# Performance work log

Hardware: AMD Instinct MI355X
Metric: run time of the kernel (lower is better)

The kernel has to match this reference:

```python
import jax, jax.numpy as jnp
import numpy as np

SMOOTH_COEF = 0.025
FLOOR = 1e-06
B, T, C = 64, 4096, 128


def setup_inputs() -> dict:
    key = jax.random.key(0)
    k1, = jax.random.split(key, 1)
    inputs = jax.random.uniform(k1, (B, T, C), dtype=jnp.float32)  # nonneg spectrogram-like
    alpha = jnp.full((C,), 0.98, dtype=jnp.float32)
    delta = jnp.full((C,), 2.0, dtype=jnp.float32)
    root = jnp.full((C,), 2.0, dtype=jnp.float32)
    return {"inputs": inputs, "alpha": alpha, "delta": delta, "root": root}


def _ema(x, s):
    # m_t = s*x_t + (1-s)*m_{t-1}, with h_{-1} = x_0 => m_0 = x_0.
    # Linear recurrence via associative scan: pairs (a_t, b_t), m_t = a_t*m_{t-1} + b_t.
    Bn, Tn, Cn = x.shape
    a = jnp.full((Tn,), 1.0 - s, dtype=x.dtype).at[0].set(0.0)
    a = jnp.broadcast_to(a[None, :, None], x.shape)
    b = (s * x).at[:, 0, :].set(x[:, 0, :])

    def comb(c1, c2):
        a1, b1 = c1
        a2, b2 = c2
        return (a1 * a2, a2 * b1 + b2)

    _, m = jax.lax.associative_scan(comb, (a, b), axis=1)
    return m


def reference(inputs, alpha, delta, root):
    alpha_c = jnp.minimum(alpha, 1.0)          # [C]
    root_c = jnp.maximum(root, 1.0)            # [C]
    m = _ema(inputs, SMOOTH_COEF)              # [B,T,C] EMA smoother
    one_over_root = 1.0 / root_c
    term1 = jnp.power(FLOOR + m, alpha_c)
    term2 = jnp.power(inputs / term1 + delta, one_over_root)
    term3 = jnp.power(delta, one_over_root)
    return term2 - term3
```

## Files before the change

kernel.cpp:

```cpp
#include <hip/hip_runtime.h>


constexpr int Bn = 64, Tn = 4096, Cn = 128;
constexpr int L = 256;
constexpr int H = 256;
constexpr int NC = Tn / L;
constexpr int RS = Cn / 2;
constexpr float SC  = 0.025f;
constexpr float OMS = 1.0f - SC;
constexpr float FLOORV = 1e-6f;

__device__ __forceinline__ float pcen1(float x, float m, float al, float dl,
                                       float oor, float t3) {
    float inv1 = exp2f(-al * log2f(FLOORV + m));
    float base = fmaf(x, inv1, dl);
    return exp2f(oor * log2f(base)) - t3;
}

__global__ __launch_bounds__(256) void k_pcen(const float* __restrict__ x,
                                              const float* __restrict__ alpha,
                                              const float* __restrict__ delta,
                                              const float* __restrict__ root,
                                              float* __restrict__ out) {
    int gid   = blockIdx.x * 256 + threadIdx.x;
    int cg    = gid & 63;
    int chunk = (gid >> 6) & (NC - 1);
    int b     = gid >> 10;

    float2 alv = *(const float2*)(alpha + 2 * cg);
    float2 dlv = *(const float2*)(delta + 2 * cg);
    float2 rtv = *(const float2*)(root  + 2 * cg);
    float a0 = fminf(alv.x, 1.f), a1 = fminf(alv.y, 1.f);
    float r0 = fmaxf(rtv.x, 1.f), r1 = fmaxf(rtv.y, 1.f);
    float o0 = 1.f / r0, o1 = 1.f / r1;
    float t30 = exp2f(o0 * log2f(dlv.x));
    float t31 = exp2f(o1 * log2f(dlv.y));

    size_t base = (size_t)b * Tn * RS + cg;
    const float2* xb = (const float2*)x  + base + (size_t)(chunk * L) * RS;
    float2*       ob = (float2*)out      + base + (size_t)(chunk * L) * RS;

    float mx, my;
    if (chunk == 0) {
        float2 v = xb[0];
        mx = v.x; my = v.y;
    } else {
        const float2* xh = xb - (size_t)H * RS;
        mx = 0.f; my = 0.f;
#pragma unroll 16
        for (int t = 0; t < H; ++t) {
            float2 v = xh[(size_t)t * RS];
            mx = fmaf(OMS, mx, SC * v.x);
            my = fmaf(OMS, my, SC * v.y);
        }
    }

#pragma unroll 8
    for (int t = 0; t < L; ++t) {
        float2 v = xb[(size_t)t * RS];
        mx = fmaf(OMS, mx, SC * v.x);
        my = fmaf(OMS, my, SC * v.y);
        float2 o;
        o.x = pcen1(v.x, mx, a0, dlv.x, o0, t30);
        o.y = pcen1(v.y, my, a1, dlv.y, o1, t31);
        ob[(size_t)t * RS] = o;
    }
}

extern "C" void kernel_launch(void* const* d_in, const int* in_sizes, int n_in,
                              void* d_out, int out_size, void* d_ws, size_t ws_size,
                              hipStream_t stream) {
    const float* x     = (const float*)d_in[0];
    const float* alpha = (const float*)d_in[1];
    const float* delta = (const float*)d_in[2];
    const float* root  = (const float*)d_in[3];
    float* out = (float*)d_out;

    const int total = Bn * NC * (Cn / 2);
    k_pcen<<<total / 256, 256, 0, stream>>>(x, alpha, delta, root, out);
}
```

Before: 281.3 us.

## Use one thread per channel with shorter chunks, sqrt fast path and nontemporal stores

Each thread now handles a single channel instead of a float2 pair, and the time chunk shrinks to 128 with a 192-step EMA warm-up, doubling thread count. Early chunks compute the exact EMA prefix. When root is 2 the power is replaced with sqrtf, and outputs use nontemporal stores. The aim is more parallelism and cheaper transcendentals, at the cost of a larger warm-up-to-chunk ratio (more redundant reads) and a shorter warm-up that loosens the EMA approximation.

Result: slower. 318.3 us (+13.2%).

```diff
diff --git a/kernel.cpp b/kernel.cpp
--- a/kernel.cpp
+++ b/kernel.cpp
@@ -2,20 +2,12 @@
 
 
 constexpr int Bn = 64, Tn = 4096, Cn = 128;
-constexpr int L = 256;
-constexpr int H = 256;
+constexpr int L = 128;
+constexpr int H = 192;
 constexpr int NC = Tn / L;
-constexpr int RS = Cn / 2;
 constexpr float SC  = 0.025f;
 constexpr float OMS = 1.0f - SC;
 constexpr float FLOORV = 1e-6f;
-
-__device__ __forceinline__ float pcen1(float x, float m, float al, float dl,
-                                       float oor, float t3) {
-    float inv1 = exp2f(-al * log2f(FLOORV + m));
-    float base = fmaf(x, inv1, dl);
-    return exp2f(oor * log2f(base)) - t3;
-}
 
 __global__ __launch_bounds__(256) void k_pcen(const float* __restrict__ x,
                                               const float* __restrict__ alpha,
@@ -23,47 +15,46 @@
                                               const float* __restrict__ root,
                                               float* __restrict__ out) {
     int gid   = blockIdx.x * 256 + threadIdx.x;
-    int cg    = gid & 63;
-    int chunk = (gid >> 6) & (NC - 1);
-    int b     = gid >> 10;
+    int ch    = gid & (Cn - 1);
+    int chunk = (gid >> 7) & (NC - 1);
+    int b     = gid >> 12;
 
-    float2 alv = *(const float2*)(alpha + 2 * cg);
-    float2 dlv = *(const float2*)(delta + 2 * cg);
-    float2 rtv = *(const float2*)(root  + 2 * cg);
-    float a0 = fminf(alv.x, 1.f), a1 = fminf(alv.y, 1.f);
-    float r0 = fmaxf(rtv.x, 1.f), r1 = fmaxf(rtv.y, 1.f);
-    float o0 = 1.f / r0, o1 = 1.f / r1;
-    float t30 = exp2f(o0 * log2f(dlv.x));
-    float t31 = exp2f(o1 * log2f(dlv.y));
+    float al = fminf(alpha[ch], 1.f);
+    float dl = delta[ch];
+    float rt = fmaxf(root[ch], 1.f);
+    float oor = 1.f / rt;
+    bool  use_sqrt = (oor == 0.5f);
+    float t3 = use_sqrt ? sqrtf(dl) : exp2f(oor * log2f(dl));
 
-    size_t base = (size_t)b * Tn * RS + cg;
-    const float2* xb = (const float2*)x  + base + (size_t)(chunk * L) * RS;
-    float2*       ob = (float2*)out      + base + (size_t)(chunk * L) * RS;
+    int start = chunk * L;
+    const float* xrow = x + (size_t)b * Tn * Cn + ch;
+    const float* xb   = xrow + (size_t)start * Cn;
+    float*       ob   = out + (size_t)b * Tn * Cn + ch + (size_t)start * Cn;
 
-    float mx, my;
-    if (chunk == 0) {
-        float2 v = xb[0];
-        mx = v.x; my = v.y;
+    float m;
+    if (start == 0) {
+        m = xb[0];
+    } else if (start <= H) {
+        m = xrow[0];
+        for (int t = 1; t < start; ++t)
+            m = fmaf(OMS, m, SC * xrow[(size_t)t * Cn]);
     } else {
-        const float2* xh = xb - (size_t)H * RS;
-        mx = 0.f; my = 0.f;
+        const float* xh = xb - (size_t)H * Cn;
+        m = 0.f;
 #pragma unroll 16
-        for (int t = 0; t < H; ++t) {
-            float2 v = xh[(size_t)t * RS];
-            mx = fmaf(OMS, mx, SC * v.x);
-            my = fmaf(OMS, my, SC * v.y);
-        }
+        for (int t = 0; t < H; ++t)
+            m = fmaf(OMS, m, SC * xh[(size_t)t * Cn]);
     }
 
 #pragma unroll 8
     for (int t = 0; t < L; ++t) {
-        float2 v = xb[(size_t)t * RS];
-        mx = fmaf(OMS, mx, SC * v.x);
-        my = fmaf(OMS, my, SC * v.y);
-        float2 o;
-        o.x = pcen1(v.x, mx, a0, dlv.x, o0, t30);
-        o.y = pcen1(v.y, my, a1, dlv.y, o1, t31);
-        ob[(size_t)t * RS] = o;
+        float v = xb[(size_t)t * Cn];
+        m = fmaf(OMS, m, SC * v);
+        float inv1 = exp2f(-al * log2f(m + FLOORV));
+        float base = fmaf(v, inv1, dl);
+        float r = (use_sqrt ? sqrtf(base)
+                            : exp2f(oor * log2f(base))) - t3;
+        __builtin_nontemporal_store(r, ob + (size_t)t * Cn);
     }
 }
 
@@ -76,6 +67,6 @@
     const float* root  = (const float*)d_in[3];
     float* out = (float*)d_out;
 
-    const int total = Bn * NC * (Cn / 2);
+    const int total = Bn * NC * Cn;
     k_pcen<<<total / 256, 256, 0, stream>>>(x, alpha, delta, root, out);
 }
```
